# Kernel optimization log

Hardware: AMD Instinct MI355X
Metric: run time of the kernel (lower is better)

Reference implementation:

```python
import jax, jax.numpy as jnp
import numpy as np

# Static config (matches init_kwargs)
VOCAB, EMBED, HIDDEN = 32000, 256, 512
SLOTS, MEM_DIM, HEADS, TOPK = 1024, 64, 4, 8
B, T = 16, 128
# beta_read/beta_write are learned scalars but the torch forward detaches them
# via .item(); treat as constants (|beta| + 1e-6 with beta init ~1.0).
BETA_R = 1.0 + 1e-6
BETA_W = 1.0 + 1e-6
EPS = 1e-8


def setup_inputs() -> dict:
    key = jax.random.key(0)
    ks = jax.random.split(key, 16)
    s = 0.02
    HD = HEADS * MEM_DIM
    return {
        "input_seq": jax.random.randint(ks[0], (B, T), 0, VOCAB),
        "E": jax.random.normal(ks[1], (VOCAB, EMBED), jnp.float32) * s,
        "W_ih": jax.random.normal(ks[2], (4 * HIDDEN, EMBED + MEM_DIM), jnp.float32) * s,
        "W_hh": jax.random.normal(ks[3], (4 * HIDDEN, HIDDEN), jnp.float32) * s,
        "b_ih": jnp.zeros((4 * HIDDEN,), jnp.float32),
        "b_hh": jnp.zeros((4 * HIDDEN,), jnp.float32),
        "W_out": jax.random.normal(ks[4], (HIDDEN, VOCAB), jnp.float32) * s,
        "b_out": jnp.zeros((VOCAB,), jnp.float32),
        "W_rk": jax.random.normal(ks[5], (HIDDEN, HD), jnp.float32) * s,
        "b_rk": jnp.zeros((HD,), jnp.float32),
        "W_wk": jax.random.normal(ks[6], (HIDDEN, HD), jnp.float32) * s,
        "b_wk": jnp.zeros((HD,), jnp.float32),
        "W_wv": jax.random.normal(ks[7], (HIDDEN, HD), jnp.float32) * s,
        "b_wv": jnp.zeros((HD,), jnp.float32),
        "W_er": jax.random.normal(ks[8], (HIDDEN, HD), jnp.float32) * s,
        "b_er": jnp.zeros((HD,), jnp.float32),
    }


def _address(memory, keys, beta):
    # memory: [B,S,D], keys: [B,H,D] -> sparse (top-k) content weights [B,H,S]
    mem_n = memory / (jnp.linalg.norm(memory, axis=-1, keepdims=True) + EPS)
    key_n = keys / (jnp.linalg.norm(keys, axis=-1, keepdims=True) + EPS)
    scores = beta * jnp.einsum("bhd,bsd->bhs", key_n, mem_n)
    vals, idx = jax.lax.top_k(scores, TOPK)           # [B,H,K]
    sm = jax.nn.softmax(vals, axis=-1)                # softmax over top-k only
    w = jnp.zeros_like(scores)
    b_ix = jnp.arange(scores.shape[0])[:, None, None]
    h_ix = jnp.arange(HEADS)[None, :, None]
    return w.at[b_ix, h_ix, idx].set(sm)              # [B,H,S]


def reference(input_seq, E, W_ih, W_hh, b_ih, b_hh, W_out, b_out,
              W_rk, b_rk, W_wk, b_wk, W_wv, b_wv, W_er, b_er):
    Bq = input_seq.shape[0]
    memory0 = jnp.full((Bq, SLOTS, MEM_DIM), 1e-6, jnp.float32)
    h0 = jnp.zeros((Bq, HIDDEN), jnp.float32)
    c0 = jnp.zeros((Bq, HIDDEN), jnp.float32)
    r0 = jnp.zeros((Bq, MEM_DIM), jnp.float32)

    def step(carry, x_t):
        memory, h, c, read_vec = carry
        emb = E[x_t]                                          # [B,embed]
        inp = jnp.concatenate([emb, read_vec], axis=-1)
        gates = inp @ W_ih.T + b_ih + h @ W_hh.T + b_hh       # [B,4H]
        i, f, g, o = jnp.split(gates, 4, axis=-1)             # torch LSTM order
        c = jax.nn.sigmoid(f) * c + jax.nn.sigmoid(i) * jnp.tanh(g)
        h = jax.nn.sigmoid(o) * jnp.tanh(c)
        logits = h @ W_out + b_out                            # [B,V]
        rk = (h @ W_rk + b_rk).reshape(Bq, HEADS, MEM_DIM)
        wk = (h @ W_wk + b_wk).reshape(Bq, HEADS, MEM_DIM)
        wv = (h @ W_wv + b_wv).reshape(Bq, HEADS, MEM_DIM)
        er = jax.nn.sigmoid(h @ W_er + b_er).reshape(Bq, HEADS, MEM_DIM)
        # content-addressed top-k read
        rw = _address(memory, rk, BETA_R)                     # [B,H,S]
        read_vec = jnp.einsum("bhs,bsd->bhd", rw, memory).mean(axis=1)
        # erase + add write
        ww = _address(memory, wk, BETA_W)                     # [B,H,S]
        keep = jnp.prod(1.0 - ww[..., None] * er[:, :, None, :], axis=1)
        add = jnp.einsum("bhs,bhd->bsd", ww, wv)
        memory = memory * keep + add
        return (memory, h, c, read_vec), logits

    _, logits_seq = jax.lax.scan(step, (memory0, h0, c0, r0), input_seq.T)
    return jnp.transpose(logits_seq, (1, 0, 2))               # [B,T,V]
```

## Files before the change

### kernel.cpp

```cpp
#include <hip/hip_runtime.h>
#include <hip/hip_bf16.h>
#include <stdint.h>

typedef unsigned int uint;
typedef unsigned long long u64;

#define T_STEPS 128
#define BQ 16
#define HID 512
#define NSLOT 1024
#define MD 64
#define VOCAB 32000
#define BETA 1.000001f
#define EPSN 1e-8f

#define NWK 128
#define NBT 16

#define LF_FH(b)  ((b)*32)
#define LF_FP(w)  ((16+(w))*32)
#define LF_FC(w)  ((48+(w))*32)
#define LF_FRV(b) ((176+(b))*32)
#define LF_FG(w)  ((192+(w))*32)
#define NLINES    320

#define AL4(dst, p) asm volatile("global_load_dwordx4 %0, %1, off sc0 sc1" : "=v"(dst) : "v"(p))
#define ALF(dst, p) asm volatile("global_load_dword %0, %1, off sc0 sc1" : "=v"(dst) : "v"(p))
#define AWAIT() do { asm volatile("s_waitcnt vmcnt(0)" ::: "memory"); __builtin_amdgcn_sched_barrier(0); } while(0)
#define DRAIN() asm volatile("s_waitcnt vmcnt(0)" ::: "memory")

__device__ __forceinline__ float sigm(float x){ return 1.f/(1.f+expf(-x)); }
__device__ __forceinline__ void astoref(float* p, float v){
  __hip_atomic_store(p, v, __ATOMIC_RELAXED, __HIP_MEMORY_SCOPE_AGENT);
}
__device__ __forceinline__ void astoreu32(uint* p, uint v){
  __hip_atomic_store(p, v, __ATOMIC_RELAXED, __HIP_MEMORY_SCOPE_AGENT);
}
__device__ __forceinline__ void astoreu64(u64* p, u64 v){
  __hip_atomic_store(p, v, __ATOMIC_RELAXED, __HIP_MEMORY_SCOPE_AGENT);
}
__device__ __forceinline__ u64 aloadu64(const u64* p){
  return __hip_atomic_load((u64*)p, __ATOMIC_RELAXED, __HIP_MEMORY_SCOPE_AGENT);
}
__device__ __forceinline__ uint aloadu32(const uint* p){
  return __hip_atomic_load((uint*)p, __ATOMIC_RELAXED, __HIP_MEMORY_SCOPE_AGENT);
}
__device__ __forceinline__ void poll1(const uint* p, uint gen){
  while (aloadu32(p) < gen) __builtin_amdgcn_s_sleep(2);
}

__device__ __forceinline__ u64 packsc(float v, int slot){
  uint u = __float_as_uint(v);
  u = (u & 0x80000000u) ? ~u : (u | 0x80000000u);
  return ((u64)u << 10) | (u64)(1023 - slot);
}
__device__ __forceinline__ float unpackval(u64 p){
  uint u = (uint)(p >> 10);
  uint bits = (u & 0x80000000u) ? (u & 0x7fffffffu) : ~u;
  return __uint_as_float(bits);
}
__device__ __forceinline__ int unpackslot(u64 p){ return 1023 - (int)(p & 1023u); }

#define L_MEM  0
#define L_NRM  8704
#define L_HS   8832
#define L_KEY  17088
#define L_KNRM 17600
#define L_SC   17608
#define L_WV   18632
#define L_ER   18888
#define L_WL   19144
#define L_RVS  19208
#define L_WTS  20232
#define L_TOT  21256

__global__ __launch_bounds__(256) void prep_emb(const float* __restrict__ E,
                                                const int* __restrict__ seq,
                                                float* __restrict__ EMB){
  int m = blockIdx.x, t = m >> 4, b = m & 15;
  int x = seq[b*T_STEPS + t];
  EMB[(size_t)m*256 + threadIdx.x] = E[(size_t)x*256 + threadIdx.x];
}

__global__ __launch_bounds__(256) void gemm_emb(const float* __restrict__ A,
                                                const float* __restrict__ W_ih,
                                                const float* __restrict__ b_ih,
                                                const float* __restrict__ b_hh,
                                                float* __restrict__ C){
  __shared__ __align__(16) float As[16*68];
  __shared__ __align__(16) float Bs[16*68];
  int mt = blockIdx.x & 31, nt = blockIdx.x >> 5;
  int m0 = mt*64, n0 = nt*64;
  int tx = threadIdx.x & 15, ty = threadIdx.x >> 4;
  float acc[4][4] = {};
  for (int k0 = 0; k0 < 256; k0 += 16){
    int mm = threadIdx.x >> 2, kq = (threadIdx.x & 3)*4;
    float4 a = *(const float4*)(A + (size_t)(m0+mm)*256 + k0 + kq);
    As[(kq+0)*68+mm]=a.x; As[(kq+1)*68+mm]=a.y; As[(kq+2)*68+mm]=a.z; As[(kq+3)*68+mm]=a.w;
    int pp = n0 + mm;
    int r = (pp & 3)*512 + (pp >> 2);
    float4 bv = *(const float4*)(W_ih + (size_t)r*320 + k0 + kq);
    Bs[(kq+0)*68+mm]=bv.x; Bs[(kq+1)*68+mm]=bv.y; Bs[(kq+2)*68+mm]=bv.z; Bs[(kq+3)*68+mm]=bv.w;
    __syncthreads();
    #pragma unroll
    for (int kk = 0; kk < 16; ++kk){
      float4 av = *(const float4*)(As + kk*68 + ty*4);
      float4 bb = *(const float4*)(Bs + kk*68 + tx*4);
      float aa[4] = {av.x,av.y,av.z,av.w};
      float bv2[4] = {bb.x,bb.y,bb.z,bb.w};
      #pragma unroll
      for (int i = 0; i < 4; ++i)
        #pragma unroll
        for (int j = 0; j < 4; ++j)
          acc[i][j] = fmaf(aa[i], bv2[j], acc[i][j]);
    }
    __syncthreads();
  }
  #pragma unroll
  for (int i = 0; i < 4; ++i){
    int m = m0 + ty*4 + i;
    #pragma unroll
    for (int j = 0; j < 4; ++j){
      int pp = n0 + tx*4 + j;
      int r = (pp & 3)*512 + (pp >> 2);
      C[(size_t)m*2048 + pp] = acc[i][j] + b_ih[r] + b_hh[r];
    }
  }
}

__global__ __launch_bounds__(256) void make_wrvT(const float* __restrict__ W_ih,
                                                 float* __restrict__ WT){
  int idx = blockIdx.x*256 + threadIdx.x;
  int k = idx >> 11, p = idx & 2047;
  int r = (p & 3)*512 + (p >> 2);
  WT[idx] = W_ih[(size_t)r*320 + 256 + k];
}

__global__ __launch_bounds__(256) void recur_kernel(
    const float* __restrict__ W_hh, const float* __restrict__ WT,
    const float* __restrict__ W_rk, const float* __restrict__ b_rk,
    const float* __restrict__ W_wk, const float* __restrict__ b_wk,
    const float* __restrict__ W_wv, const float* __restrict__ b_wv,
    const float* __restrict__ W_er, const float* __restrict__ b_er,
    const float* __restrict__ G_emb, float* __restrict__ H_all,
    float* __restrict__ H_pub, float* __restrict__ mem_g,
    float* __restrict__ projpub, float* __restrict__ gatespub,
    float* __restrict__ rvpub, u64* __restrict__ cand,
    u64* __restrict__ wlist, uint* __restrict__ arrv)
{
  __shared__ __align__(16) float smem[L_TOT];
  const int tid = threadIdx.x;
  const int wg  = blockIdx.x;

  if (wg < NWK){
    float* mem_s  = smem + L_MEM;
    float* nrm_s  = smem + L_NRM;
    float* hs     = smem + L_HS;
    float* key_s  = smem + L_KEY;
    float* knrm_s = smem + L_KNRM;
    float* sc_s   = smem + L_SC;
    float* wv_s   = smem + L_WV;
    float* er_s   = smem + L_ER;
    u64*   wl_s   = (u64*)(smem + L_WL);
    float* rv_s   = smem + L_RVS;
    float* WT_s   = smem + L_WTS;

    const int b_s = wg >> 3, rg = wg & 7, s0 = rg*128;
    const int gb = tid >> 4, gc = tid & 15;
    const int pcol = wg*16 + gc;
    const int rrow = (pcol & 3)*512 + (pcol >> 2);
    float* mslice_g = mem_g + ((size_t)b_s*NSLOT + s0)*MD;
    const float* W1 = (wg < 16) ? W_rk : W_wk;
    const float* B1 = (wg < 16) ? b_rk : b_wk;
    const float* W2 = (wg < 16) ? W_wv : W_er;
    const float* B2 = (wg < 16) ? b_wv : b_er;
    const int cc = (wg & 15)*16 + gc;
    const float pb1 = (wg < 32) ? B1[cc] : 0.f;
    const float pb2 = (wg < 32) ? B2[cc] : 0.f;

    for (int i = tid; i < 64*16; i += 256){
      int d = i >> 4, c = i & 15;
      WT_s[i] = WT[(size_t)d*2048 + wg*16 + c];
    }
    for (int i = tid; i < 128*MD; i += 256){
      mem_s[(i >> 6)*68 + (i & 63)] = 1e-6f;
      astoref(mslice_g + i, 1e-6f);
    }
    __syncthreads();
    {
      int s = tid >> 1, half = tid & 1;
      const float4* mp = (const float4*)(mem_s + s*68 + half*32);
      float sum = 0.f;
      #pragma unroll
      for (int q = 0; q < 8; ++q){
        float4 v = mp[q];
        sum = fmaf(v.x,v.x,sum); sum = fmaf(v.y,v.y,sum);
        sum = fmaf(v.z,v.z,sum); sum = fmaf(v.w,v.w,sum);
      }
      sum += __shfl_xor(sum, 1);
      if (half == 0) nrm_s[s] = sqrtf(sum) + EPSN;
    }
    __syncthreads();

    #pragma clang loop unroll(disable)
    for (int t = 0; t < T_STEPS-1; ++t){
      const int par = t & 1, parp = par ^ 1;
      if (t > 0){
        if (tid < 32) wl_s[tid] = aloadu64(wlist + (size_t)b_s*32 + tid);
        if (tid < 64){
          float4 v; AL4(v, (const float4*)(projpub + (size_t)parp*BQ*1024 + (size_t)b_s*1024 + 512) + tid);
          AWAIT();
          *(float4*)(wv_s + tid*4) = v;
        } else if (tid < 128){
          int i = tid - 64;
          float4 v; AL4(v, (const float4*)(projpub + (size_t)parp*BQ*1024 + (size_t)b_s*1024 + 768) + i);
          AWAIT();
          *(float4*)(er_s + i*4) = v;
        }
        __syncthreads();
        if (tid < 64){
          const int d = tid;
          #pragma unroll 1
          for (int e = 0; e < 32; ++e){
            u64 w64 = wl_s[e];
            int sl = (int)(w64 & 0xffffffffu);
            if (sl >= s0 && sl < s0+128){
              float w = __uint_as_float((uint)(w64 >> 32));
              mem_s[(sl-s0)*68 + d] *= (1.f - w*er_s[(e >> 3)*64 + d]);
            }
          }
          #pragma unroll 1
          for (int e = 0; e < 32; ++e){
            u64 w64 = wl_s[e];
            int sl = (int)(w64 & 0xffffffffu);
            if (sl >= s0 && sl < s0+128){
              float w = __uint_as_float((uint)(w64 >> 32));
              mem_s[(sl-s0)*68 + d] += w*wv_s[(e >> 3)*64 + d];
            }
          }
          #pragma unroll 1
          for (int e = 0; e < 32; ++e){
            u64 w64 = wl_s[e];
            int sl = (int)(w64 & 0xffffffffu);
            if (sl >= s0 && sl < s0+128)
              astoref(mslice_g + (sl-s0)*MD + d, mem_s[(sl-s0)*68 + d]);
          }
        }
        __syncthreads();
        {
          int s = tid >> 1, half = tid & 1;
          const float4* mp = (const float4*)(mem_s + s*68 + half*32);
          float sum = 0.f;
          #pragma unroll
          for (int q = 0; q < 8; ++q){
            float4 v = mp[q];
            sum = fmaf(v.x,v.x,sum); sum = fmaf(v.y,v.y,sum);
            sum = fmaf(v.z,v.z,sum); sum = fmaf(v.w,v.w,sum);
          }
          sum += __shfl_xor(sum, 1);
          if (half == 0) nrm_s[s] = sqrtf(sum) + EPSN;
        }
      }
      if (tid < 16) poll1(arrv + LF_FH(tid), (uint)(t+1));
      __syncthreads();
      {
        float4 v0,v1,v2,v3,v4,v5,v6,v7;
        const float4* hp = (const float4*)H_pub;
        AL4(v0, hp + tid);        AL4(v1, hp + tid + 256);
        AL4(v2, hp + tid + 512);  AL4(v3, hp + tid + 768);
        AL4(v4, hp + tid + 1024); AL4(v5, hp + tid + 1280);
        AL4(v6, hp + tid + 1536); AL4(v7, hp + tid + 1792);
        AWAIT();
        int i;
        i = tid;        *(float4*)(hs + (i>>7)*516 + (i&127)*4) = v0;
        i = tid + 256;  *(float4*)(hs + (i>>7)*516 + (i&127)*4) = v1;
        i = tid + 512;  *(float4*)(hs + (i>>7)*516 + (i&127)*4) = v2;
        i = tid + 768;  *(float4*)(hs + (i>>7)*516 + (i&127)*4) = v3;
        i = tid + 1024; *(float4*)(hs + (i>>7)*516 + (i&127)*4) = v4;
        i = tid + 1280; *(float4*)(hs + (i>>7)*516 + (i&127)*4) = v5;
        i = tid + 1536; *(float4*)(hs + (i>>7)*516 + (i&127)*4) = v6;
        i = tid + 1792; *(float4*)(hs + (i>>7)*516 + (i&127)*4) = v7;
      }
      __syncthreads();
      if (wg < 32){
        float a0=0.f,a1=0.f,b0=0.f,b1=0.f;
        const float* hp = hs + gb*516;
        const float* w1 = W1 + cc;
        const float* w2 = W2 + cc;
        #pragma unroll 4
        for (int k = 0; k < 512; k += 2){
          float h0 = hp[k], h1 = hp[k+1];
          a0 = fmaf(h0, w1[(size_t)k*256], a0);
          b0 = fmaf(h0, w2[(size_t)k*256], b0);
          a1 = fmaf(h1, w1[(size_t)(k+1)*256], a1);
          b1 = fmaf(h1, w2[(size_t)(k+1)*256], b1);
        }
        float v1 = a0 + a1 + pb1;
        float v2 = b0 + b1 + pb2;
        if (wg >= 16) v2 = sigm(v2);
        astoref(projpub + (size_t)par*BQ*1024 + (size_t)gb*1024 + wg*16 + gc, v1);
        astoref(projpub + (size_t)par*BQ*1024 + (size_t)gb*1024 + 512 + wg*16 + gc, v2);
      }
      DRAIN();
      __syncthreads();
      if (wg < 32 && tid == 0) astoreu32(arrv + LF_FP(wg), (uint)(t+1));
      if (tid < 32) poll1(arrv + LF_FP(tid), (uint)(t+1));
      __syncthreads();
      if (tid < 128){
        float4 kv; AL4(kv, (const float4*)(projpub + (size_t)par*BQ*1024 + (size_t)b_s*1024) + tid);
        AWAIT();
        *(float4*)(key_s + tid*4) = kv;
      }
      __syncthreads();
      if (tid < 8){
        const float4* kp = (const float4*)(key_s + tid*MD);
        float sum = 0.f;
        #pragma unroll
        for (int q = 0; q < 16; ++q){
          float4 v = kp[q];
          sum = fmaf(v.x,v.x,sum); sum = fmaf(v.y,v.y,sum);
          sum = fmaf(v.z,v.z,sum); sum = fmaf(v.w,v.w,sum);
        }
        knrm_s[tid] = sqrtf(sum) + EPSN;
      }
      __syncthreads();
      {
        int s = tid >> 1, kh = tid & 1;
        const float4* mp = (const float4*)(mem_s + s*68);
        float rnm = 1.f / nrm_s[s];
        float acc4[4] = {0.f,0.f,0.f,0.f};
        #pragma unroll
        for (int q = 0; q < 16; ++q){
          float4 m = mp[q];
          #pragma unroll
          for (int kk = 0; kk < 4; ++kk){
            float4 k4 = *(const float4*)(key_s + (kh*4+kk)*MD + q*4);
            acc4[kk] = fmaf(m.x,k4.x,acc4[kk]); acc4[kk] = fmaf(m.y,k4.y,acc4[kk]);
            acc4[kk] = fmaf(m.z,k4.z,acc4[kk]); acc4[kk] = fmaf(m.w,k4.w,acc4[kk]);
          }
        }
        #pragma unroll
        for (int kk = 0; kk < 4; ++kk){
          int key = kh*4 + kk;
          sc_s[key*128 + s] = BETA * acc4[kk] * rnm / knrm_s[key];
        }
      }
      __syncthreads();
      {
        int wid = tid >> 6, lane = tid & 63;
        #pragma unroll
        for (int kk = 0; kk < 2; ++kk){
          int key = wid*2 + kk;
          u64 p0 = packsc(sc_s[key*128 + lane],      s0 + lane);
          u64 p1 = packsc(sc_s[key*128 + 64 + lane], s0 + 64 + lane);
          #pragma unroll
          for (int r = 0; r < 8; ++r){
            u64 m = p0 > p1 ? p0 : p1;
            #pragma unroll
            for (int o = 32; o; o >>= 1){ u64 q = __shfl_xor(m, o); if (q > m) m = q; }
            if (p0 == m) p0 = 0; else if (p1 == m) p1 = 0;
            if (lane == 0) astoreu64(cand + (((size_t)b_s*8 + key)*8 + rg)*8 + r, m);
          }
        }
      }
      DRAIN();
      __syncthreads();
      if (tid == 0) astoreu32(arrv + LF_FC(wg), (uint)(t+1));
      float gpv;
      {
        float a0 = G_emb[(size_t)((t+1)*BQ + gb)*2048 + pcol];
        float a1 = 0.f, a2 = 0.f, a3 = 0.f;
        const float4* wh = (const float4*)(W_hh + (size_t)rrow*HID);
        const float4* xv = (const float4*)(hs + gb*516);
        #pragma unroll 2
        for (int k = 0; k < 128; k += 4){
          float4 w, x;
          w=wh[k+0]; x=xv[k+0]; a0=fmaf(w.x,x.x,a0); a0=fmaf(w.y,x.y,a0); a0=fmaf(w.z,x.z,a0); a0=fmaf(w.w,x.w,a0);
          w=wh[k+1]; x=xv[k+1]; a1=fmaf(w.x,x.x,a1); a1=fmaf(w.y,x.y,a1); a1=fmaf(w.z,x.z,a1); a1=fmaf(w.w,x.w,a1);
          w=wh[k+2]; x=xv[k+2]; a2=fmaf(w.x,x.x,a2); a2=fmaf(w.y,x.y,a2); a2=fmaf(w.z,x.z,a2); a2=fmaf(w.w,x.w,a2);
          w=wh[k+3]; x=xv[k+3]; a3=fmaf(w.x,x.x,a3); a3=fmaf(w.y,x.y,a3); a3=fmaf(w.z,x.z,a3); a3=fmaf(w.w,x.w,a3);
        }
        gpv = (a0+a1)+(a2+a3);
      }
      if (tid < 16) poll1(arrv + LF_FRV(tid), (uint)(t+1));
      __syncthreads();
      {
        float4 v; AL4(v, (const float4*)rvpub + tid); AWAIT();
        *(float4*)(rv_s + tid*4) = v;
      }
      __syncthreads();
      {
        float acc = gpv;
        #pragma unroll 8
        for (int d = 0; d < 64; ++d)
          acc = fmaf(rv_s[gb*64 + d], WT_s[d*16 + gc], acc);
        astoref(gatespub + (size_t)gb*2048 + pcol, acc);
      }
      DRAIN();
      __syncthreads();
      if (tid == 0) astoreu32(arrv + LF_FG(wg), (uint)(t+1));
    }
  } else {
    const int b = wg - NWK;
    float* rv_st = smem;
    float c0, c1;
    {
      float4 gA = *(const float4*)(G_emb + (size_t)b*2048 + tid*8);
      float4 gB = *(const float4*)(G_emb + (size_t)b*2048 + tid*8 + 4);
      c0 = sigm(gA.x)*tanhf(gA.z);
      float h0v = sigm(gA.w)*tanhf(c0);
      c1 = sigm(gB.x)*tanhf(gB.z);
      float h1v = sigm(gB.w)*tanhf(c1);
      astoref(H_pub + (size_t)b*HID + tid*2,     h0v);
      astoref(H_pub + (size_t)b*HID + tid*2 + 1, h1v);
      H_all[(size_t)b*HID + tid*2]     = h0v;
      H_all[(size_t)b*HID + tid*2 + 1] = h1v;
    }
    DRAIN();
    __syncthreads();
    if (tid == 0) astoreu32(arrv + LF_FH(b), 1u);

    #pragma clang loop unroll(disable)
    for (int t = 0; t < T_STEPS-1; ++t){
      if (tid < 8) poll1(arrv + LF_FC(b*8 + tid), (uint)(t+1));
      __syncthreads();
      {
        int wid = tid >> 6, lane = tid & 63;
        #pragma unroll
        for (int kk = 0; kk < 2; ++kk){
          int key = wid*2 + kk;
          u64 pv = aloadu64(cand + (((size_t)b*8 + key)*8 + (lane >> 3))*8 + (lane & 7));
          u64 sel = 0;
          #pragma unroll
          for (int r = 0; r < 8; ++r){
            u64 m = pv;
            #pragma unroll
            for (int o = 32; o; o >>= 1){ u64 q = __shfl_xor(m, o); if (q > m) m = q; }
            if (pv == m) pv = 0;
            if (lane == r) sel = m;
          }
          float val = unpackval(sel);
          int slot = unpackslot(sel);
          float vmax = __shfl(val, 0);
          float e = (lane < 8) ? expf(val - vmax) : 0.f;
          float ssum = e;
          #pragma unroll
          for (int o = 32; o; o >>= 1) ssum += __shfl_xor(ssum, o);
          float w = e / ssum;
          if (key < 4){
            int sls[8];
            #pragma unroll
            for (int i = 0; i < 8; ++i) sls[i] = __shfl(slot, i);
            float mv[8];
            #pragma unroll
            for (int i = 0; i < 8; ++i)
              ALF(mv[i], mem_g + ((size_t)b*NSLOT + sls[i])*MD + lane);
            AWAIT();
            float acc = 0.f;
            #pragma unroll
            for (int i = 0; i < 8; ++i) acc = fmaf(__shfl(w, i), mv[i], acc);
            rv_st[key*64 + lane] = acc;
          } else if (lane < 8){
            astoreu64(wlist + (size_t)b*32 + (key-4)*8 + lane,
                      ((u64)__float_as_uint(w) << 32) | (u64)(uint)slot);
          }
        }
      }
      __syncthreads();
      if (tid < 64){
        float m = 0.25f*(rv_st[tid] + rv_st[64+tid] + rv_st[128+tid] + rv_st[192+tid]);
        astoref(rvpub + (size_t)b*MD + tid, m);
      }
      DRAIN();
      __syncthreads();
      if (tid == 0) astoreu32(arrv + LF_FRV(b), (uint)(t+1));
      if (tid < 128) poll1(arrv + LF_FG(tid), (uint)(t+1));
      __syncthreads();
      {
        float4 gA, gB;
        AL4(gA, (const float4*)(gatespub + (size_t)b*2048) + tid*2);
        AL4(gB, (const float4*)(gatespub + (size_t)b*2048) + tid*2 + 1);
        AWAIT();
        c0 = sigm(gA.y)*c0 + sigm(gA.x)*tanhf(gA.z);
        float h0v = sigm(gA.w)*tanhf(c0);
        c1 = sigm(gB.y)*c1 + sigm(gB.x)*tanhf(gB.z);
        float h1v = sigm(gB.w)*tanhf(c1);
        astoref(H_pub + (size_t)b*HID + tid*2,     h0v);
        astoref(H_pub + (size_t)b*HID + tid*2 + 1, h1v);
        H_all[(size_t)((t+1)*BQ + b)*HID + tid*2]     = h0v;
        H_all[(size_t)((t+1)*BQ + b)*HID + tid*2 + 1] = h1v;
      }
      DRAIN();
      __syncthreads();
      if (tid == 0) astoreu32(arrv + LF_FH(b), (uint)(t+2));
    }
  }
}

__global__ __launch_bounds__(256) void gemm_out(const float* __restrict__ A,
                                                const float* __restrict__ Bmat,
                                                const float* __restrict__ bias,
                                                float* __restrict__ C){
  __shared__ __align__(16) float As[16*132];
  __shared__ __align__(16) float Bs[16*64];
  int mt = blockIdx.x & 15, nt = blockIdx.x >> 4;
  int m0 = mt*128, n0 = nt*64;
  int tx = threadIdx.x & 15, ty = threadIdx.x >> 4;
  float acc[8][4] = {};
  for (int k0 = 0; k0 < 512; k0 += 16){
    int mm = threadIdx.x >> 1, kq = (threadIdx.x & 1)*8;
    float4 a0 = *(const float4*)(A + (size_t)(m0+mm)*512 + k0 + kq);
    float4 a1 = *(const float4*)(A + (size_t)(m0+mm)*512 + k0 + kq + 4);
    As[(kq+0)*132+mm]=a0.x; As[(kq+1)*132+mm]=a0.y; As[(kq+2)*132+mm]=a0.z; As[(kq+3)*132+mm]=a0.w;
    As[(kq+4)*132+mm]=a1.x; As[(kq+5)*132+mm]=a1.y; As[(kq+6)*132+mm]=a1.z; As[(kq+7)*132+mm]=a1.w;
    int kk2 = threadIdx.x >> 4, nq = (threadIdx.x & 15)*4;
    *(float4*)(Bs + kk2*64 + nq) = *(const float4*)(Bmat + (size_t)(k0+kk2)*VOCAB + n0 + nq);
    __syncthreads();
    #pragma unroll
    for (int kk = 0; kk < 16; ++kk){
      float4 x0 = *(const float4*)(As + kk*132 + ty*8);
      float4 x1 = *(const float4*)(As + kk*132 + ty*8 + 4);
      float4 bv = *(const float4*)(Bs + kk*64 + tx*4);
      float aa[8] = {x0.x,x0.y,x0.z,x0.w,x1.x,x1.y,x1.z,x1.w};
      float bb[4] = {bv.x,bv.y,bv.z,bv.w};
      #pragma unroll
      for (int i = 0; i < 8; ++i)
        #pragma unroll
        for (int j = 0; j < 4; ++j)
          acc[i][j] = fmaf(aa[i], bb[j], acc[i][j]);
    }
    __syncthreads();
  }
  #pragma unroll
  for (int i = 0; i < 8; ++i){
    int m = m0 + ty*8 + i;
    int bq = m & 15, tt = m >> 4;
    float* crow = C + ((size_t)bq*T_STEPS + tt)*VOCAB + n0 + tx*4;
    #pragma unroll
    for (int j = 0; j < 4; ++j) crow[j] = acc[i][j] + bias[n0 + tx*4 + j];
  }
}

extern "C" void kernel_launch(void* const* d_in, const int* in_sizes, int n_in,
                              void* d_out, int out_size, void* d_ws, size_t ws_size,
                              hipStream_t stream){
  const int*   seq   = (const int*)d_in[0];
  const float* E     = (const float*)d_in[1];
  const float* W_ih  = (const float*)d_in[2];
  const float* W_hh  = (const float*)d_in[3];
  const float* b_ih  = (const float*)d_in[4];
  const float* b_hh  = (const float*)d_in[5];
  const float* W_out = (const float*)d_in[6];
  const float* b_out = (const float*)d_in[7];
  const float* W_rk  = (const float*)d_in[8];
  const float* b_rk  = (const float*)d_in[9];
  const float* W_wk  = (const float*)d_in[10];
  const float* b_wk  = (const float*)d_in[11];
  const float* W_wv  = (const float*)d_in[12];
  const float* b_wv  = (const float*)d_in[13];
  const float* W_er  = (const float*)d_in[14];
  const float* b_er  = (const float*)d_in[15];
  float* out = (float*)d_out;
  (void)in_sizes; (void)n_in; (void)out_size; (void)ws_size;

  char* ws = (char*)d_ws;
  size_t off = 0;
  auto alloc = [&](size_t bytes) -> void* {
    off = (off + 255) & ~(size_t)255;
    void* p = ws + off;
    off += bytes;
    return p;
  };
  float* EMB      = (float*)alloc((size_t)2048*256*4);
  float* G_emb    = (float*)alloc((size_t)2048*2048*4);
  float* H_all    = (float*)alloc((size_t)2048*512*4);
  float* H_pub    = (float*)alloc((size_t)16*512*4);
  float* mem_g    = (float*)alloc((size_t)16*1024*64*4);
  float* projpub  = (float*)alloc((size_t)2*16*1024*4);
  float* gatespub = (float*)alloc((size_t)16*2048*4);
  float* rvpub    = (float*)alloc((size_t)16*64*4);
  u64*   cand     = (u64*)alloc((size_t)16*8*8*8*8);
  u64*   wlist    = (u64*)alloc((size_t)16*32*8);
  float* WT       = (float*)alloc((size_t)64*2048*4);
  uint*  arrv     = (uint*)alloc((size_t)NLINES*32*4);

  hipMemsetAsync(arrv, 0, (size_t)NLINES*32*4, stream);
  prep_emb<<<2048, 256, 0, stream>>>(E, seq, EMB);
  gemm_emb<<<1024, 256, 0, stream>>>(EMB, W_ih, b_ih, b_hh, G_emb);
  make_wrvT<<<512, 256, 0, stream>>>(W_ih, WT);
  recur_kernel<<<NWK + NBT, 256, 0, stream>>>(
      W_hh, WT, W_rk, b_rk, W_wk, b_wk, W_wv, b_wv, W_er, b_er,
      G_emb, H_all, H_pub, mem_g, projpub, gatespub, rvpub, cand, wlist, arrv);
  gemm_out<<<16*500, 256, 0, stream>>>(H_all, W_out, b_out, out);
}
```

Measured before the change: 7.006 ms.

## Run output projection on bf16 MFMA with hi/lo split for fp32 accuracy

Replaces the scalar fp32 output GEMM (H_all × W_out) with a matrix-core kernel. It splits both operands into bf16 high and low parts and accumulates four MFMA products per tile, which keeps close to fp32 accuracy. W_out is transposed and split in a kernel launched before the recurrence, and H_all is split after it. The aim is to move the 32000-wide projection off the vector ALUs; the costs are extra workspace, extra split passes over memory, and a fallback to the old kernel if the workspace is too small.

```diff
diff --git a/kernel.cpp b/kernel.cpp
--- a/kernel.cpp
+++ b/kernel.cpp
@@ -3,7 +3,10 @@
 #include <stdint.h>
 
 typedef unsigned int uint;
+typedef unsigned short ushort;
 typedef unsigned long long u64;
+typedef __attribute__((ext_vector_type(8))) short s8v;
+typedef __attribute__((ext_vector_type(4))) float f4v;
 
 #define T_STEPS 128
 #define BQ 16
@@ -60,6 +63,15 @@
   return __uint_as_float(bits);
 }
 __device__ __forceinline__ int unpackslot(u64 p){ return 1023 - (int)(p & 1023u); }
+
+__device__ __forceinline__ ushort f2bf(float x){
+  __hip_bfloat16 h = __float2bfloat16(x);
+  return *(ushort*)&h;
+}
+__device__ __forceinline__ float bf2f(ushort u){
+  __hip_bfloat16 h; *(ushort*)&h = u;
+  return __bfloat162float(h);
+}
 
 #define L_MEM  0
 #define L_NRM  8704
@@ -134,6 +146,37 @@
   int k = idx >> 11, p = idx & 2047;
   int r = (p & 3)*512 + (p >> 2);
   WT[idx] = W_ih[(size_t)r*320 + 256 + k];
+}
+
+__global__ __launch_bounds__(256) void split_BT(const float* __restrict__ W,
+                                                ushort* __restrict__ BThi,
+                                                ushort* __restrict__ BTlo){
+  __shared__ float tl[32][33];
+  int kt = blockIdx.x & 15, nt = blockIdx.x >> 4;
+  int k0 = kt*32, n0 = nt*32;
+  int tx = threadIdx.x & 31, ty = threadIdx.x >> 5;
+  #pragma unroll
+  for (int i = 0; i < 4; ++i)
+    tl[ty + i*8][tx] = W[(size_t)(k0 + ty + i*8)*VOCAB + n0 + tx];
+  __syncthreads();
+  #pragma unroll
+  for (int i = 0; i < 4; ++i){
+    float x = tl[tx][ty + i*8];
+    ushort hi = f2bf(x);
+    ushort lo = f2bf(x - bf2f(hi));
+    size_t o = (size_t)(n0 + ty + i*8)*512 + k0 + tx;
+    BThi[o] = hi; BTlo[o] = lo;
+  }
+}
+
+__global__ __launch_bounds__(256) void split_A(const float* __restrict__ H,
+                                               ushort* __restrict__ Ahi,
+                                               ushort* __restrict__ Alo){
+  int idx = blockIdx.x*256 + threadIdx.x;
+  float x = H[idx];
+  ushort hi = f2bf(x);
+  Ahi[idx] = hi;
+  Alo[idx] = f2bf(x - bf2f(hi));
 }
 
 __global__ __launch_bounds__(256) void recur_kernel(
@@ -497,6 +540,87 @@
   }
 }
 
+#define GM_NT 250
+__global__ __launch_bounds__(256) void gemm_mfma(
+    const ushort* __restrict__ Ahi, const ushort* __restrict__ Alo,
+    const ushort* __restrict__ BThi, const ushort* __restrict__ BTlo,
+    const float* __restrict__ bias, float* __restrict__ C)
+{
+  __shared__ __align__(16) ushort ldsu[4*128*40];
+  const int tid = threadIdx.x;
+  int mt = blockIdx.x / GM_NT, nt = blockIdx.x - mt*GM_NT;
+  int m0 = mt*128, n0 = nt*128;
+  const int wv = tid >> 6, lane = tid & 63;
+  const int wm = (wv & 1)*64, wn = (wv >> 1)*64;
+  const int fr = lane & 15, kh = (lane >> 4)*8;
+
+  f4v acc[4][4];
+  #pragma unroll
+  for (int i = 0; i < 4; ++i)
+    #pragma unroll
+    for (int j = 0; j < 4; ++j)
+      acc[i][j] = (f4v){0.f,0.f,0.f,0.f};
+
+  const int sr = tid & 127, sel = tid >> 7;
+  const ushort* srcA = (sel ? Alo : Ahi) + (size_t)(m0 + sr)*512;
+  const ushort* srcB = (sel ? BTlo : BThi) + (size_t)(n0 + sr)*512;
+  ushort* dstA = ldsu + (size_t)sel*5120 + sr*40;
+  ushort* dstB = ldsu + (size_t)(2+sel)*5120 + sr*40;
+
+  for (int ks = 0; ks < 16; ++ks){
+    const int k0 = ks*32;
+    __syncthreads();
+    {
+      uint4 a0 = *(const uint4*)(srcA + k0);
+      uint4 a1 = *(const uint4*)(srcA + k0 + 8);
+      uint4 a2 = *(const uint4*)(srcA + k0 + 16);
+      uint4 a3 = *(const uint4*)(srcA + k0 + 24);
+      uint4 b0 = *(const uint4*)(srcB + k0);
+      uint4 b1 = *(const uint4*)(srcB + k0 + 8);
+      uint4 b2 = *(const uint4*)(srcB + k0 + 16);
+      uint4 b3 = *(const uint4*)(srcB + k0 + 24);
+      *(uint4*)(dstA +  0) = a0; *(uint4*)(dstA +  8) = a1;
+      *(uint4*)(dstA + 16) = a2; *(uint4*)(dstA + 24) = a3;
+      *(uint4*)(dstB +  0) = b0; *(uint4*)(dstB +  8) = b1;
+      *(uint4*)(dstB + 16) = b2; *(uint4*)(dstB + 24) = b3;
+    }
+    __syncthreads();
+    s8v ah[4], al[4], bh[4], bl[4];
+    #pragma unroll
+    for (int mi = 0; mi < 4; ++mi){
+      ah[mi] = *(const s8v*)(ldsu + 0*5120 + (wm + mi*16 + fr)*40 + kh);
+      al[mi] = *(const s8v*)(ldsu + 1*5120 + (wm + mi*16 + fr)*40 + kh);
+    }
+    #pragma unroll
+    for (int ni = 0; ni < 4; ++ni){
+      bh[ni] = *(const s8v*)(ldsu + 2*5120 + (wn + ni*16 + fr)*40 + kh);
+      bl[ni] = *(const s8v*)(ldsu + 3*5120 + (wn + ni*16 + fr)*40 + kh);
+    }
+    #pragma unroll
+    for (int mi = 0; mi < 4; ++mi)
+      #pragma unroll
+      for (int ni = 0; ni < 4; ++ni){
+        acc[mi][ni] = __builtin_amdgcn_mfma_f32_16x16x32_bf16(ah[mi], bh[ni], acc[mi][ni], 0, 0, 0);
+        acc[mi][ni] = __builtin_amdgcn_mfma_f32_16x16x32_bf16(ah[mi], bl[ni], acc[mi][ni], 0, 0, 0);
+        acc[mi][ni] = __builtin_amdgcn_mfma_f32_16x16x32_bf16(al[mi], bh[ni], acc[mi][ni], 0, 0, 0);
+        acc[mi][ni] = __builtin_amdgcn_mfma_f32_16x16x32_bf16(al[mi], bl[ni], acc[mi][ni], 0, 0, 0);
+      }
+  }
+  #pragma unroll
+  for (int ni = 0; ni < 4; ++ni){
+    int col = n0 + wn + ni*16 + fr;
+    float bz = bias[col];
+    #pragma unroll
+    for (int mi = 0; mi < 4; ++mi){
+      #pragma unroll
+      for (int j = 0; j < 4; ++j){
+        int row = m0 + wm + mi*16 + (lane >> 4)*4 + j;
+        C[((size_t)(row & 15)*T_STEPS + (row >> 4))*VOCAB + col] = acc[mi][ni][j] + bz;
+      }
+    }
+  }
+}
+
 __global__ __launch_bounds__(256) void gemm_out(const float* __restrict__ A,
                                                 const float* __restrict__ Bmat,
                                                 const float* __restrict__ bias,
@@ -561,7 +685,7 @@
   const float* W_er  = (const float*)d_in[14];
   const float* b_er  = (const float*)d_in[15];
   float* out = (float*)d_out;
-  (void)in_sizes; (void)n_in; (void)out_size; (void)ws_size;
+  (void)in_sizes; (void)n_in; (void)out_size;
 
   char* ws = (char*)d_ws;
   size_t off = 0;
@@ -583,13 +707,25 @@
   u64*   wlist    = (u64*)alloc((size_t)16*32*8);
   float* WT       = (float*)alloc((size_t)64*2048*4);
   uint*  arrv     = (uint*)alloc((size_t)NLINES*32*4);
+  ushort* Ahi  = (ushort*)alloc((size_t)2048*512*2);
+  ushort* Alo  = (ushort*)alloc((size_t)2048*512*2);
+  ushort* BThi = (ushort*)alloc((size_t)VOCAB*512*2);
+  ushort* BTlo = (ushort*)alloc((size_t)VOCAB*512*2);
+  const bool use_mfma = (off <= ws_size);
 
   hipMemsetAsync(arrv, 0, (size_t)NLINES*32*4, stream);
   prep_emb<<<2048, 256, 0, stream>>>(E, seq, EMB);
   gemm_emb<<<1024, 256, 0, stream>>>(EMB, W_ih, b_ih, b_hh, G_emb);
   make_wrvT<<<512, 256, 0, stream>>>(W_ih, WT);
+  if (use_mfma)
+    split_BT<<<16000, 256, 0, stream>>>(W_out, BThi, BTlo);
   recur_kernel<<<NWK + NBT, 256, 0, stream>>>(
       W_hh, WT, W_rk, b_rk, W_wk, b_wk, W_wv, b_wv, W_er, b_er,
       G_emb, H_all, H_pub, mem_g, projpub, gatespub, rvpub, cand, wlist, arrv);
-  gemm_out<<<16*500, 256, 0, stream>>>(H_all, W_out, b_out, out);
-}
+  if (use_mfma){
+    split_A<<<4096, 256, 0, stream>>>(H_all, Ahi, Alo);
+    gemm_mfma<<<16*GM_NT, 256, 0, stream>>>(Ahi, Alo, BThi, BTlo, b_out, out);
+  } else {
+    gemm_out<<<16*500, 256, 0, stream>>>(H_all, W_out, b_out, out);
+  }
+}
```

After: 6.497 ms. 7.3% less time.
